# Optimization experiments

Measured on AMD Instinct MI355X. Metric: run time of the kernel, lower is better.

Reference implementation:

```python
import jax, jax.numpy as jnp
import numpy as np

ITER_NUM = 3       # nSteps of the SICE proximal loop (module iterNum)
NS_ITERS = 7       # Newton-Schulz iterations, hardcoded in _sice
F_LR = 5.0         # sice_lrate
F_SPARSITY = 0.07  # sparsity_val
BN_EPS = 1e-5


def _inv_sqrtm(x, iterN):
    """Batched Newton-Schulz inverse matrix square root (Sqrtm.forward)."""
    d = x.shape[-1]
    I3 = 3.0 * jnp.eye(d, dtype=x.dtype)
    normA = jnp.trace(x, axis1=-2, axis2=-1)            # [B]
    A = x / normA[:, None, None]
    ZY = 0.5 * (I3 - A)
    Y = A @ ZY
    Z = ZY
    for _ in range(iterN - 2):
        ZY = 0.5 * (I3 - Z @ Y)
        Y = Y @ ZY
        Z = ZY @ Z
    ZYZ = 0.5 * (I3 - Z @ Y) @ Z
    return ZYZ * (normA ** -0.5)[:, None, None]


def _covpool(x):
    """x: [B,C,H,W] -> centered second-order pooling [B,C,C] (Covpool)."""
    b, c, h, w = x.shape
    m = h * w
    xf = x.reshape(b, c, m)
    xc = xf - xf.mean(axis=-1, keepdims=True)
    # x @ I_hat @ x^T == (x - mean)(x - mean)^T / M
    return (xc @ xc.transpose(0, 2, 1)) / m


def _sice(x, jitter):
    C = _covpool(x)
    C = C / jnp.trace(C, axis1=-2, axis2=-1)[:, None, None]
    Ij = jnp.diag(1e-10 + 1e-9 * jitter)[None].astype(C.dtype)   # [1,D,D]
    zz = _inv_sqrtm(C + Ij, NS_ITERS)
    LLT = zz @ zz                                                # inv covariance init
    sym_C = 0.5 * (C + C.transpose(0, 2, 1))
    for i in range(ITER_NUM):
        Lp = jax.nn.relu(LLT)
        Lm = jax.nn.relu(-LLT)
        zz = _inv_sqrtm(LLT + Ij, NS_ITERS)
        g12 = -(zz @ zz) + sym_C
        dec = F_LR * (1.0 - i / (ITER_NUM - 1.0))
        Lp = jax.nn.relu(Lp - dec * (g12 + F_SPARSITY))
        Lm = jax.nn.relu(Lm - dec * (-g12 + F_SPARSITY))
        LLT = Lp - Lm
        LLT = 0.5 * (LLT + LLT.transpose(0, 2, 1))
    return LLT / jnp.sqrt(jnp.trace(LLT, axis1=-2, axis2=-1))[:, None, None]


def reference(x, conv_w, gamma, beta, jitter):
    # 1x1 conv dimension reduction + BatchNorm (batch stats, train mode) + ReLU
    y = jnp.einsum('bchw,dc->bdhw', x, conv_w)
    mu = y.mean(axis=(0, 2, 3), keepdims=True)
    var = y.var(axis=(0, 2, 3), keepdims=True)
    y = (y - mu) / jnp.sqrt(var + BN_EPS)
    y = jax.nn.relu(y * gamma[None, :, None, None] + beta[None, :, None, None])
    out = _sice(y, jitter)                                       # [B,D,D]
    b, d = out.shape[0], out.shape[1]
    iu = np.nonzero(np.triu(np.ones((d, d))).reshape(-1))[0]     # Triuvec indices
    return out.reshape(b, d * d)[:, iu]                          # [B, D*(D+1)/2]


def setup_inputs() -> dict:
    key = jax.random.key(0)
    k1, k2, k3 = jax.random.split(key, 3)
    B, CIN, H, W, DR = 32, 2048, 28, 28, 256
    x = jax.random.normal(k1, (B, CIN, H, W), dtype=jnp.float32)
    # kaiming normal, mode=fan_out (fan_out = DR*1*1): std = sqrt(2/DR)
    conv_w = jax.random.normal(k2, (DR, CIN), dtype=jnp.float32) * np.sqrt(2.0 / DR).astype(np.float32)
    gamma = jnp.ones((DR,), dtype=jnp.float32)
    beta = jnp.zeros((DR,), dtype=jnp.float32)
    jitter = jax.random.uniform(k3, (DR,), dtype=jnp.float32)
    return {"x": x, "conv_w": conv_w, "gamma": gamma, "beta": beta, "jitter": jitter}
```

## Files before the change

### kernel.cpp

```cpp
#include <hip/hip_runtime.h>
#include <utility>


typedef unsigned short u16;
typedef __attribute__((ext_vector_type(8))) __bf16 bf16x8;
typedef __attribute__((ext_vector_type(8))) _Float16 f16x8;
typedef __attribute__((ext_vector_type(4))) float f32x4;

#define DEV __device__ __forceinline__

DEV u16 f2bf(float f) {
  unsigned x = __float_as_uint(f);
  x += 0x7fffu + ((x >> 16) & 1u);
  return (u16)(x >> 16);
}
DEV float bf2f(u16 h) { return __uint_as_float(((unsigned)h) << 16); }

#define SB_SUM   0
#define SB_SSQ   256
#define SB_IJ    512
#define SB_TRC   768
#define SB_TR2   800
#define SB_TR3   832
#define SB_TRL   864
#define SB_DEN   896
#define SB_IJSUM 928

__global__ __launch_bounds__(256) void k_prep(const float* __restrict__ w,
                                              const float* __restrict__ jitter,
                                              _Float16* __restrict__ w_half,
                                              float* __restrict__ sb) {
  int gid = blockIdx.x * 256 + threadIdx.x;
  if (gid < 256 * 2048) w_half[gid] = (_Float16)w[gid];
  if (blockIdx.x == 0) {
    int t = threadIdx.x;
    float ij = 1e-10f + 1e-9f * jitter[t];
    sb[SB_IJ + t] = ij;
    if (t < 160) sb[SB_TRC + t] = 0.f;
    __shared__ float red[256];
    red[t] = ij; __syncthreads();
    for (int off = 128; off > 0; off >>= 1) {
      if (t < off) red[t] += red[t + off];
      __syncthreads();
    }
    if (t == 0) sb[SB_IJSUM] = red[0];
  }
}

__global__ __launch_bounds__(256) void k_conv(const _Float16* __restrict__ w_half,
                                              const float* __restrict__ x,
                                              _Float16* __restrict__ y) {
  int xb = blockIdx.x;
  int b = xb & 31;
  int rest = xb >> 5;
  int mt = rest / 13, ht = rest % 13;
  int hw0 = ht * 64;
  int t = threadIdx.x;
  int wv = t >> 6, lane = t & 63, m = lane & 15, quad = lane >> 4;
  __shared__ _Float16 lsA[2][128 * 40];
  __shared__ _Float16 lsB[2][64 * 40];
  f32x4 acc[4][2];
#pragma unroll
  for (int i = 0; i < 4; ++i)
#pragma unroll
    for (int j = 0; j < 2; ++j) acc[i][j] = (f32x4){0.f, 0.f, 0.f, 0.f};
  int rowA = t & 127, halfA = t >> 7;
  const _Float16* wp = w_half + ((size_t)(mt * 128 + rowA)) * 2048 + halfA * 16;
  int hwB = t & 63, cg = t >> 6;
  bool okB = (hw0 + hwB) < 784;
  const float* xp = x + ((size_t)b * 2048 + cg * 8) * 784 + hw0 + hwB;
  uint4 ra0, ra1;
  float rb[8];
  ra0 = *(const uint4*)(wp);
  ra1 = *(const uint4*)(wp + 8);
#pragma unroll
  for (int j = 0; j < 8; ++j) rb[j] = okB ? xp[(size_t)j * 784] : 0.f;
  int wr = (wv >> 1) * 64, wc = (wv & 1) * 32;
  for (int kc = 0; kc < 64; ++kc) {
    int buf = kc & 1;
    int loA = rowA * 40 + halfA * 16;
    *(uint4*)&lsA[buf][loA] = ra0;
    *(uint4*)&lsA[buf][loA + 8] = ra1;
    {
      union { f16x8 h; uint4 u; } pk;
#pragma unroll
      for (int j = 0; j < 8; ++j) pk.h[j] = (_Float16)rb[j];
      *(uint4*)&lsB[buf][hwB * 40 + cg * 8] = pk.u;
    }
    if (kc < 63) {
      int k0 = (kc + 1) * 32;
      ra0 = *(const uint4*)(wp + k0);
      ra1 = *(const uint4*)(wp + k0 + 8);
#pragma unroll
      for (int j = 0; j < 8; ++j)
        rb[j] = okB ? xp[((size_t)k0 + j) * 784] : 0.f;
    }
    __syncthreads();
    f16x8 af[4], bfg[2];
#pragma unroll
    for (int i = 0; i < 4; ++i)
      af[i] = *(const f16x8*)&lsA[buf][(wr + i * 16 + m) * 40 + quad * 8];
#pragma unroll
    for (int j = 0; j < 2; ++j)
      bfg[j] = *(const f16x8*)&lsB[buf][(wc + j * 16 + m) * 40 + quad * 8];
#pragma unroll
    for (int i = 0; i < 4; ++i)
#pragma unroll
      for (int j = 0; j < 2; ++j)
        acc[i][j] = __builtin_amdgcn_mfma_f32_16x16x32_f16(af[i], bfg[j], acc[i][j], 0, 0, 0);
  }
#pragma unroll
  for (int i = 0; i < 4; ++i)
#pragma unroll
    for (int j = 0; j < 2; ++j)
#pragma unroll
      for (int r = 0; r < 4; ++r) {
        int R = mt * 128 + wr + i * 16 + quad * 4 + r;
        int hwc = hw0 + wc + j * 16 + m;
        if (hwc < 784) y[((size_t)b * 256 + R) * 784 + hwc] = (_Float16)acc[i][j][r];
      }
}

__global__ __launch_bounds__(256) void k_stats(const _Float16* __restrict__ y,
                                               float* __restrict__ sb) {
  int d = blockIdx.x, t = threadIdx.x;
  float s = 0.f, q = 0.f;
  if (t < 196) {
    for (int b = 0; b < 32; ++b) {
      const _Float16* row = y + ((size_t)b * 256 + d) * 784;
      union { uint2 u; _Float16 h[4]; } v;
      v.u = *(const uint2*)(row + t * 4);
#pragma unroll
      for (int k = 0; k < 4; ++k) {
        float f = (float)v.h[k];
        s += f; q += f * f;
      }
    }
  }
  __shared__ float rs[256], rq[256];
  rs[t] = s; rq[t] = q; __syncthreads();
  for (int off = 128; off > 0; off >>= 1) {
    if (t < off) { rs[t] += rs[t + off]; rq[t] += rq[t + off]; }
    __syncthreads();
  }
  if (t == 0) { sb[SB_SUM + d] = rs[0]; sb[SB_SSQ + d] = rq[0]; }
}

__global__ __launch_bounds__(256) void k_bnapply(const _Float16* __restrict__ y,
                                                 const float* __restrict__ gamma,
                                                 const float* __restrict__ beta,
                                                 const float* __restrict__ sb,
                                                 _Float16* __restrict__ yc) {
  int xb = blockIdx.x;
  int d = xb >> 5, b = xb & 31, t = threadIdx.x;
  float mu = sb[SB_SUM + d] * (1.0f / 25088.0f);
  float var = sb[SB_SSQ + d] * (1.0f / 25088.0f) - mu * mu;
  float sc = gamma[d] / sqrtf(var + 1e-5f);
  float sh = beta[d] - mu * sc;
  const _Float16* row = y + ((size_t)b * 256 + d) * 784;
  float v[4];
  float s = 0.f;
#pragma unroll
  for (int i = 0; i < 4; ++i) {
    int idx = t + i * 256;
    float u = 0.f;
    if (idx < 784) u = fmaxf((float)row[idx] * sc + sh, 0.f);
    v[i] = u; s += u;
  }
  __shared__ float red[256];
  red[t] = s; __syncthreads();
  for (int off = 128; off > 0; off >>= 1) {
    if (t < off) red[t] += red[t + off];
    __syncthreads();
  }
  float mean = red[0] * (1.0f / 784.0f);
  _Float16* out = yc + ((size_t)b * 256 + d) * 800;
#pragma unroll
  for (int i = 0; i < 4; ++i) {
    int idx = t + i * 256;
    if (idx < 784) out[idx] = (_Float16)(v[i] - mean);
  }
  if (t < 16) out[784 + t] = (_Float16)0.f;
}

__global__ __launch_bounds__(256) void k_gram(const _Float16* __restrict__ yc,
                                              float* __restrict__ C,
                                              float* __restrict__ sb) {
  int xb = blockIdx.x;
  int b = xb & 31, rest = xb >> 5;
  int tr = rest >> 2, tc = rest & 3;
  int t = threadIdx.x, wv = t >> 6, lane = t & 63, m = lane & 15, quad = lane >> 4;
  __shared__ _Float16 lsA[2][32 * 40];
  __shared__ _Float16 lsB[2][64 * 40];
  f32x4 acc[2];
  acc[0] = (f32x4){0.f, 0.f, 0.f, 0.f};
  acc[1] = (f32x4){0.f, 0.f, 0.f, 0.f};
  int row = t >> 2, seg = t & 3;
  const _Float16* base = yc + (size_t)b * 256 * 800;
  const _Float16* Bp = base + (size_t)(tc * 64 + row) * 800 + seg * 8;
  const _Float16* Ap = base + (size_t)(tr * 32 + row) * 800 + seg * 8;
  bool doA = row < 32;
  uint4 rB = *(const uint4*)(Bp);
  uint4 rA = doA ? *(const uint4*)(Ap) : (uint4){0, 0, 0, 0};
  int ar = (wv >> 1) * 16, bcl = (wv & 1) * 32;
  for (int ks = 0; ks < 25; ++ks) {
    int buf = ks & 1;
    int lo = row * 40 + seg * 8;
    *(uint4*)&lsB[buf][lo] = rB;
    if (doA) *(uint4*)&lsA[buf][lo] = rA;
    if (ks < 24) {
      int k0 = (ks + 1) * 32;
      rB = *(const uint4*)(Bp + k0);
      if (doA) rA = *(const uint4*)(Ap + k0);
    }
    __syncthreads();
    f16x8 a0 = *(const f16x8*)&lsA[buf][(ar + m) * 40 + quad * 8];
    f16x8 b0 = *(const f16x8*)&lsB[buf][(bcl + m) * 40 + quad * 8];
    f16x8 b1 = *(const f16x8*)&lsB[buf][(bcl + 16 + m) * 40 + quad * 8];
    acc[0] = __builtin_amdgcn_mfma_f32_16x16x32_f16(a0, b0, acc[0], 0, 0, 0);
    acc[1] = __builtin_amdgcn_mfma_f32_16x16x32_f16(a0, b1, acc[1], 0, 0, 0);
  }
  const float inv = 1.0f / 784.0f;
#pragma unroll
  for (int j = 0; j < 2; ++j)
#pragma unroll
    for (int r = 0; r < 4; ++r) {
      int R = tr * 32 + ar + quad * 4 + r;
      int Cc = tc * 64 + bcl + j * 16 + m;
      float v = acc[j][r] * inv;
      C[((size_t)b * 256 + R) * 256 + Cc] = v;
      if (R == Cc) atomicAdd(&sb[SB_TRC + b], v);
    }
}

__global__ __launch_bounds__(256) void k_prepAZY(const float* __restrict__ src,
                                                 float* __restrict__ symC,
                                                 u16* __restrict__ Ah, u16* __restrict__ Al,
                                                 u16* __restrict__ ZYh, u16* __restrict__ ZYl,
                                                 float* __restrict__ sb, int slot, int mode) {
  int xb = blockIdx.x;
  int ig = xb >> 5, b = xb & 31, j = threadIdx.x;
  float trv = (mode == 0) ? 1.0f : sb[slot + b];
  float denom = trv + sb[SB_IJSUM];
  if (ig == 0 && j == 0) sb[SB_DEN + b] = denom;
  float trC = (mode == 0) ? sb[SB_TRC + b] : 1.0f;
#pragma unroll
  for (int ii = 0; ii < 8; ++ii) {
    int i = ig * 8 + ii;
    size_t idx = ((size_t)b * 256 + i) * 256 + j;
    float v;
    if (mode == 0) {
      float vij = src[idx] / trC;
      float vji = src[((size_t)b * 256 + j) * 256 + i] / trC;
      symC[idx] = 0.5f * (vij + vji);
      v = vij;
    } else {
      v = src[idx];
    }
    if (i == j) v += sb[SB_IJ + i];
    float A = v / denom;
    u16 h = f2bf(A);
    Ah[idx] = h; Al[idx] = f2bf(A - bf2f(h));
    float zy = 0.5f * ((i == j ? 3.0f : 0.0f) - A);
    h = f2bf(zy);
    ZYh[idx] = h; ZYl[idx] = f2bf(zy - bf2f(h));
  }
}

struct MMArgs {
  const u16* Ah; const u16* Al; const u16* Bh;
  u16* Oh; u16* Ol; float* Of; float* tr; int emode;
};

__global__ __launch_bounds__(256) void mm_ns(MMArgs g0, MMArgs g1,
                                             const float* __restrict__ sb) {
  int xb = blockIdx.x;
  int b = xb & 31;
  int rest = xb >> 5;
  MMArgs g = (rest < 32) ? g0 : g1;
  int tile = rest & 31;
  int tr = tile >> 2, tc = tile & 3;
  int t = threadIdx.x, wv = t >> 6, lane = t & 63, m = lane & 15, quad = lane >> 4;
  __shared__ u16 lsAh[2][32 * 40], lsAl[2][32 * 40];
  __shared__ u16 lsBh[2][64 * 40];
  f32x4 acc[2];
  acc[0] = (f32x4){0.f, 0.f, 0.f, 0.f};
  acc[1] = (f32x4){0.f, 0.f, 0.f, 0.f};
  int row = t >> 2, seg = t & 3;
  size_t mb = (size_t)b * 65536;
  size_t bO = mb + (size_t)(tc * 64 + row) * 256 + seg * 8;
  size_t aO = mb + (size_t)(tr * 32 + row) * 256 + seg * 8;
  bool doA = row < 32;
  uint4 rBh = *(const uint4*)(g.Bh + bO);
  uint4 rAh = doA ? *(const uint4*)(g.Ah + aO) : (uint4){0, 0, 0, 0};
  uint4 rAl = doA ? *(const uint4*)(g.Al + aO) : (uint4){0, 0, 0, 0};
  int ar = (wv >> 1) * 16, bcl = (wv & 1) * 32;
  for (int ks = 0; ks < 8; ++ks) {
    int buf = ks & 1;
    int lo = row * 40 + seg * 8;
    *(uint4*)&lsBh[buf][lo] = rBh;
    if (doA) {
      *(uint4*)&lsAh[buf][lo] = rAh;
      *(uint4*)&lsAl[buf][lo] = rAl;
    }
    if (ks < 7) {
      int k0 = (ks + 1) * 32;
      rBh = *(const uint4*)(g.Bh + bO + k0);
      if (doA) {
        rAh = *(const uint4*)(g.Ah + aO + k0);
        rAl = *(const uint4*)(g.Al + aO + k0);
      }
    }
    __syncthreads();
    bf16x8 ah = *(const bf16x8*)&lsAh[buf][(ar + m) * 40 + quad * 8];
    bf16x8 al = *(const bf16x8*)&lsAl[buf][(ar + m) * 40 + quad * 8];
    bf16x8 bh0 = *(const bf16x8*)&lsBh[buf][(bcl + m) * 40 + quad * 8];
    bf16x8 bh1 = *(const bf16x8*)&lsBh[buf][(bcl + 16 + m) * 40 + quad * 8];
    acc[0] = __builtin_amdgcn_mfma_f32_16x16x32_bf16(ah, bh0, acc[0], 0, 0, 0);
    acc[0] = __builtin_amdgcn_mfma_f32_16x16x32_bf16(al, bh0, acc[0], 0, 0, 0);
    acc[1] = __builtin_amdgcn_mfma_f32_16x16x32_bf16(ah, bh1, acc[1], 0, 0, 0);
    acc[1] = __builtin_amdgcn_mfma_f32_16x16x32_bf16(al, bh1, acc[1], 0, 0, 0);
  }
  float scl = 1.0f;
  if (g.emode == 2) scl = 1.0f / sqrtf(sb[SB_DEN + b]);
#pragma unroll
  for (int j = 0; j < 2; ++j)
#pragma unroll
    for (int r = 0; r < 4; ++r) {
      int R = tr * 32 + ar + quad * 4 + r;
      int Cc = tc * 64 + bcl + j * 16 + m;
      float v = acc[j][r];
      if (g.emode == 1) v = 0.5f * ((R == Cc ? 3.0f : 0.0f) - v);
      else if (g.emode == 2) v = v * scl;
      size_t oidx = mb + (size_t)R * 256 + Cc;
      if (g.emode == 3) {
        g.Of[oidx] = v;
        if (R == Cc && g.tr) atomicAdd(g.tr + b, v);
      } else {
        u16 h = f2bf(v);
        g.Oh[oidx] = h;
        g.Ol[oidx] = f2bf(v - bf2f(h));
      }
    }
}

__global__ __launch_bounds__(256) void k_sice(const float* __restrict__ LLT,
                                              const float* __restrict__ P,
                                              const float* __restrict__ symC,
                                              float* __restrict__ out,
                                              float* __restrict__ sb, int slot,
                                              float dec) {
  int xb = blockIdx.x;
  int b = xb & 31, p = xb >> 5;
  const int TRt[10] = {0, 0, 0, 0, 1, 1, 1, 2, 2, 3};
  const int TCt[10] = {0, 1, 2, 3, 1, 2, 3, 2, 3, 3};
  int tr = TRt[p], tc = TCt[p];
  __shared__ float ft[64][65];
  __shared__ float ot[64][65];
  int t = threadIdx.x;
  size_t base = (size_t)b * 65536;
#pragma unroll 4
  for (int it = 0; it < 16; ++it) {
    int idx = it * 256 + t;
    int r = idx >> 6, c = idx & 63;
    size_t o = base + (size_t)(tc * 64 + r) * 256 + tr * 64 + c;
    float L = LLT[o];
    float g = symC[o] - P[o];
    float f = fmaxf(fmaxf(L, 0.f) - dec * (g + 0.07f), 0.f) -
              fmaxf(fmaxf(-L, 0.f) - dec * (-g + 0.07f), 0.f);
    ft[r][c] = f;
  }
  __syncthreads();
  float tsum = 0.f;
#pragma unroll 4
  for (int it = 0; it < 16; ++it) {
    int idx = it * 256 + t;
    int r = idx >> 6, c = idx & 63;
    size_t o = base + (size_t)(tr * 64 + r) * 256 + tc * 64 + c;
    float L = LLT[o];
    float g = symC[o] - P[o];
    float f = fmaxf(fmaxf(L, 0.f) - dec * (g + 0.07f), 0.f) -
              fmaxf(fmaxf(-L, 0.f) - dec * (-g + 0.07f), 0.f);
    float val = 0.5f * (f + ft[c][r]);
    out[o] = val;
    ot[r][c] = val;
    if (tr == tc && r == c) tsum += val;
  }
  if (tr == tc) {
    if (tsum != 0.f) atomicAdd(&sb[slot + b], tsum);
  } else {
    __syncthreads();
#pragma unroll 4
    for (int it = 0; it < 16; ++it) {
      int idx = it * 256 + t;
      int r = idx >> 6, c = idx & 63;
      size_t o = base + (size_t)(tc * 64 + r) * 256 + tr * 64 + c;
      out[o] = ot[c][r];
    }
  }
}

__global__ __launch_bounds__(256) void k_out(const float* __restrict__ LLT,
                                             const float* __restrict__ sb,
                                             float* __restrict__ out) {
  int xb = blockIdx.x;
  int i = xb >> 5, b = xb & 31, j = threadIdx.x;
  if (j < i) return;
  float inv = 1.0f / sqrtf(sb[SB_TRL + b]);
  int tl = i * 256 - (i * (i - 1)) / 2 + (j - i);
  out[(size_t)b * 32896 + tl] = LLT[((size_t)b * 256 + i) * 256 + j] * inv;
}

extern "C" void kernel_launch(void* const* d_in, const int* in_sizes, int n_in,
                              void* d_out, int out_size, void* d_ws, size_t ws_size,
                              hipStream_t stream) {
  const float* x = (const float*)d_in[0];
  const float* w = (const float*)d_in[1];
  const float* gamma = (const float*)d_in[2];
  const float* beta = (const float*)d_in[3];
  const float* jitter = (const float*)d_in[4];
  char* ws = (char*)d_ws;

  _Float16* w_half = (_Float16*)(ws + 0);
  float* sb = (float*)(ws + (1 << 20));
  _Float16* y = (_Float16*)(ws + (2 << 20));
  _Float16* yc = (_Float16*)(ws + (16 << 20));
  char* ov = ws + (32 << 20);
  float* Craw = (float*)(ov + 0);
  float* symC = (float*)(ov + 8388608);
  float* LLTa = (float*)(ov + 16777216);
  float* P = (float*)(ov + 25165824);
  float* LLTb = (float*)(ov + 33554432);
  u16* bf[12];
  for (int i = 0; i < 12; ++i) bf[i] = (u16*)(ov + 41943040 + (size_t)i * 4194304);

  k_prep<<<2048, 256, 0, stream>>>(w, jitter, w_half, sb);
  k_conv<<<832, 256, 0, stream>>>(w_half, x, y);
  k_stats<<<256, 256, 0, stream>>>(y, sb);
  k_bnapply<<<8192, 256, 0, stream>>>(y, gamma, beta, sb, yc);
  k_gram<<<1024, 256, 0, stream>>>(yc, Craw, sb);

  auto run_ns = [&](const float* src, int mode, int slot_in, float* Pout,
                    float* tr_out) {
    k_prepAZY<<<1024, 256, 0, stream>>>(src, symC, bf[0], bf[1], bf[2], bf[3], sb, slot_in, mode);
    u16 *Ah = bf[0], *Al = bf[1], *ZYh = bf[2], *ZYl = bf[3];
    u16 *Yh = bf[4], *Yl = bf[5], *Z2h = bf[6], *Z2l = bf[7];
    u16 *Th = bf[8], *Tl = bf[9], *zzh = bf[10], *zzl = bf[11];
    MMArgs m1{Ah, Al, ZYh, Yh, Yl, nullptr, nullptr, 0};
    mm_ns<<<1024, 256, 0, stream>>>(m1, m1, sb);
    u16 *Ych = Yh, *Ycl = Yl, *Yah = Ah, *Yal = Al;
    u16 *Zch = ZYh, *Zcl = ZYl, *Zah = Z2h, *Zal = Z2l;
    for (int it = 0; it < 5; ++it) {
      MMArgs mt{Zch, Zcl, Ych, Th, Tl, nullptr, nullptr, 1};
      mm_ns<<<1024, 256, 0, stream>>>(mt, mt, sb);
      MMArgs my{Ych, Ycl, Th, Yah, Yal, nullptr, nullptr, 0};
      MMArgs mz{Th, Tl, Zch, Zah, Zal, nullptr, nullptr, 0};
      mm_ns<<<2048, 256, 0, stream>>>(my, mz, sb);
      std::swap(Ych, Yah); std::swap(Ycl, Yal);
      std::swap(Zch, Zah); std::swap(Zcl, Zal);
    }
    MMArgs mt6{Zch, Zcl, Ych, Th, Tl, nullptr, nullptr, 1};
    mm_ns<<<1024, 256, 0, stream>>>(mt6, mt6, sb);
    MMArgs mz7{Th, Tl, Zch, zzh, zzl, nullptr, nullptr, 2};
    mm_ns<<<1024, 256, 0, stream>>>(mz7, mz7, sb);
    MMArgs mzz{zzh, zzl, zzh, nullptr, nullptr, Pout, tr_out, 3};
    mm_ns<<<1024, 256, 0, stream>>>(mzz, mzz, sb);
  };

  run_ns(Craw, 0, 0, LLTa, sb + SB_TR2);
  run_ns(LLTa, 1, SB_TR2, P, nullptr);
  k_sice<<<320, 256, 0, stream>>>(LLTa, P, symC, LLTb, sb, SB_TR3, 5.0f);
  run_ns(LLTb, 1, SB_TR3, P, nullptr);
  k_sice<<<320, 256, 0, stream>>>(LLTb, P, symC, LLTa, sb, SB_TRL, 2.5f);

  k_out<<<8192, 256, 0, stream>>>(LLTa, sb, (float*)d_out);
}
```

Measured before the change: 878.4 us.

## Exploit symmetry in Gram and NS matmuls; split-K conv with fused reduce-stats

The Gram kernel and every Newton-Schulz matmul now compute only the 20 upper-triangular 32x64 tiles per batch (instead of 32) and mirror results via a shared-memory transpose. This relies on the products being symmetric, which holds for commuting polynomial iterates of a symmetric matrix. The conv is restructured as split-K over four 512-channel chunks with full 256-row tiles, writing fp32 partials. A new reduce kernel sums the partials, writes fp16 y and atomically accumulates the BN statistics. This adds extra partial-sum traffic in exchange for more conv parallelism and less matmul work.

```diff
diff --git a/kernel.cpp b/kernel.cpp
--- a/kernel.cpp
+++ b/kernel.cpp
@@ -34,6 +34,8 @@
   if (gid < 256 * 2048) w_half[gid] = (_Float16)w[gid];
   if (blockIdx.x == 0) {
     int t = threadIdx.x;
+    sb[SB_SUM + t] = 0.f;
+    sb[SB_SSQ + t] = 0.f;
     float ij = 1e-10f + 1e-9f * jitter[t];
     sb[SB_IJ + t] = ij;
     if (t < 160) sb[SB_TRC + t] = 0.f;
@@ -49,92 +51,93 @@
 
 __global__ __launch_bounds__(256) void k_conv(const _Float16* __restrict__ w_half,
                                               const float* __restrict__ x,
-                                              _Float16* __restrict__ y) {
+                                              float* __restrict__ yp) {
   int xb = blockIdx.x;
   int b = xb & 31;
   int rest = xb >> 5;
-  int mt = rest / 13, ht = rest % 13;
+  int kc = rest / 13, ht = rest % 13;
   int hw0 = ht * 64;
+  int kbase = kc * 512;
   int t = threadIdx.x;
   int wv = t >> 6, lane = t & 63, m = lane & 15, quad = lane >> 4;
-  __shared__ _Float16 lsA[2][128 * 40];
-  __shared__ _Float16 lsB[2][64 * 40];
-  f32x4 acc[4][2];
+  __shared__ _Float16 lsA[256 * 40];
+  __shared__ _Float16 lsB[64 * 40];
+  f32x4 acc[4][4];
 #pragma unroll
   for (int i = 0; i < 4; ++i)
 #pragma unroll
-    for (int j = 0; j < 2; ++j) acc[i][j] = (f32x4){0.f, 0.f, 0.f, 0.f};
-  int rowA = t & 127, halfA = t >> 7;
-  const _Float16* wp = w_half + ((size_t)(mt * 128 + rowA)) * 2048 + halfA * 16;
+    for (int j = 0; j < 4; ++j) acc[i][j] = (f32x4){0.f, 0.f, 0.f, 0.f};
+  const _Float16* wp = w_half + (size_t)t * 2048 + kbase;
   int hwB = t & 63, cg = t >> 6;
   bool okB = (hw0 + hwB) < 784;
-  const float* xp = x + ((size_t)b * 2048 + cg * 8) * 784 + hw0 + hwB;
-  uint4 ra0, ra1;
+  const float* xp = x + ((size_t)b * 2048 + kbase + cg * 8) * 784 + hw0 + hwB;
+  uint4 ra[4];
   float rb[8];
-  ra0 = *(const uint4*)(wp);
-  ra1 = *(const uint4*)(wp + 8);
+#pragma unroll
+  for (int s = 0; s < 4; ++s) ra[s] = *(const uint4*)(wp + s * 8);
 #pragma unroll
   for (int j = 0; j < 8; ++j) rb[j] = okB ? xp[(size_t)j * 784] : 0.f;
-  int wr = (wv >> 1) * 64, wc = (wv & 1) * 32;
-  for (int kc = 0; kc < 64; ++kc) {
-    int buf = kc & 1;
-    int loA = rowA * 40 + halfA * 16;
-    *(uint4*)&lsA[buf][loA] = ra0;
-    *(uint4*)&lsA[buf][loA + 8] = ra1;
+  for (int it = 0; it < 16; ++it) {
+    if (it) __syncthreads();
+#pragma unroll
+    for (int s = 0; s < 4; ++s) *(uint4*)&lsA[t * 40 + s * 8] = ra[s];
     {
       union { f16x8 h; uint4 u; } pk;
 #pragma unroll
       for (int j = 0; j < 8; ++j) pk.h[j] = (_Float16)rb[j];
-      *(uint4*)&lsB[buf][hwB * 40 + cg * 8] = pk.u;
-    }
-    if (kc < 63) {
-      int k0 = (kc + 1) * 32;
-      ra0 = *(const uint4*)(wp + k0);
-      ra1 = *(const uint4*)(wp + k0 + 8);
+      *(uint4*)&lsB[hwB * 40 + cg * 8] = pk.u;
+    }
+    __syncthreads();
+    if (it < 15) {
+      int k0 = (it + 1) * 32;
+#pragma unroll
+      for (int s = 0; s < 4; ++s) ra[s] = *(const uint4*)(wp + k0 + s * 8);
 #pragma unroll
       for (int j = 0; j < 8; ++j)
         rb[j] = okB ? xp[((size_t)k0 + j) * 784] : 0.f;
     }
-    __syncthreads();
-    f16x8 af[4], bfg[2];
+    f16x8 af[4], bfg[4];
 #pragma unroll
     for (int i = 0; i < 4; ++i)
-      af[i] = *(const f16x8*)&lsA[buf][(wr + i * 16 + m) * 40 + quad * 8];
-#pragma unroll
-    for (int j = 0; j < 2; ++j)
-      bfg[j] = *(const f16x8*)&lsB[buf][(wc + j * 16 + m) * 40 + quad * 8];
+      af[i] = *(const f16x8*)&lsA[(wv * 64 + i * 16 + m) * 40 + quad * 8];
+#pragma unroll
+    for (int j = 0; j < 4; ++j)
+      bfg[j] = *(const f16x8*)&lsB[(j * 16 + m) * 40 + quad * 8];
 #pragma unroll
     for (int i = 0; i < 4; ++i)
 #pragma unroll
-      for (int j = 0; j < 2; ++j)
+      for (int j = 0; j < 4; ++j)
         acc[i][j] = __builtin_amdgcn_mfma_f32_16x16x32_f16(af[i], bfg[j], acc[i][j], 0, 0, 0);
   }
+  float* out = yp + (size_t)(kc * 32 + b) * 256 * 784;
 #pragma unroll
   for (int i = 0; i < 4; ++i)
 #pragma unroll
-    for (int j = 0; j < 2; ++j)
+    for (int j = 0; j < 4; ++j)
 #pragma unroll
       for (int r = 0; r < 4; ++r) {
-        int R = mt * 128 + wr + i * 16 + quad * 4 + r;
-        int hwc = hw0 + wc + j * 16 + m;
-        if (hwc < 784) y[((size_t)b * 256 + R) * 784 + hwc] = (_Float16)acc[i][j][r];
+        int R = wv * 64 + i * 16 + quad * 4 + r;
+        int hwc = hw0 + j * 16 + m;
+        if (hwc < 784) out[(size_t)R * 784 + hwc] = acc[i][j][r];
       }
 }
 
-__global__ __launch_bounds__(256) void k_stats(const _Float16* __restrict__ y,
-                                               float* __restrict__ sb) {
-  int d = blockIdx.x, t = threadIdx.x;
+__global__ __launch_bounds__(256) void k_red(const float* __restrict__ yp,
+                                             _Float16* __restrict__ y,
+                                             float* __restrict__ sb) {
+  int xb = blockIdx.x;
+  int b = xb & 31, d = xb >> 5, t = threadIdx.x;
+  const size_t cs = (size_t)32 * 256 * 784;
+  const float* p = yp + ((size_t)b * 256 + d) * 784;
+  _Float16* yo = y + ((size_t)b * 256 + d) * 784;
   float s = 0.f, q = 0.f;
-  if (t < 196) {
-    for (int b = 0; b < 32; ++b) {
-      const _Float16* row = y + ((size_t)b * 256 + d) * 784;
-      union { uint2 u; _Float16 h[4]; } v;
-      v.u = *(const uint2*)(row + t * 4);
-#pragma unroll
-      for (int k = 0; k < 4; ++k) {
-        float f = (float)v.h[k];
-        s += f; q += f * f;
-      }
+#pragma unroll
+  for (int it = 0; it < 4; ++it) {
+    int idx = it * 256 + t;
+    if (idx < 784) {
+      float v = p[idx] + p[cs + idx] + p[2 * cs + idx] + p[3 * cs + idx];
+      yo[idx] = (_Float16)v;
+      s += v; q += v * v;
     }
   }
   __shared__ float rs[256], rq[256];
@@ -143,7 +146,10 @@
     if (t < off) { rs[t] += rs[t + off]; rq[t] += rq[t + off]; }
     __syncthreads();
   }
-  if (t == 0) { sb[SB_SUM + d] = rs[0]; sb[SB_SSQ + d] = rq[0]; }
+  if (t == 0) {
+    atomicAdd(&sb[SB_SUM + d], rs[0]);
+    atomicAdd(&sb[SB_SSQ + d], rq[0]);
+  }
 }
 
 __global__ __launch_bounds__(256) void k_bnapply(const _Float16* __restrict__ y,
@@ -183,15 +189,19 @@
   if (t < 16) out[784 + t] = (_Float16)0.f;
 }
 
+__device__ __constant__ signed char SYM_TR[20] = {0,1,2,3,4,5,6,7, 2,3,4,5,6,7, 4,5,6,7, 6,7};
+__device__ __constant__ signed char SYM_TC[20] = {0,0,0,0,0,0,0,0, 1,1,1,1,1,1, 2,2,2,2, 3,3};
+
 __global__ __launch_bounds__(256) void k_gram(const _Float16* __restrict__ yc,
                                               float* __restrict__ C,
                                               float* __restrict__ sb) {
   int xb = blockIdx.x;
-  int b = xb & 31, rest = xb >> 5;
-  int tr = rest >> 2, tc = rest & 3;
+  int b = xb & 31, p = xb >> 5;
+  int tr = SYM_TR[p], tc = SYM_TC[p];
   int t = threadIdx.x, wv = t >> 6, lane = t & 63, m = lane & 15, quad = lane >> 4;
   __shared__ _Float16 lsA[2][32 * 40];
   __shared__ _Float16 lsB[2][64 * 40];
+  __shared__ float lsT[32][65];
   f32x4 acc[2];
   acc[0] = (f32x4){0.f, 0.f, 0.f, 0.f};
   acc[1] = (f32x4){0.f, 0.f, 0.f, 0.f};
@@ -221,16 +231,30 @@
     acc[1] = __builtin_amdgcn_mfma_f32_16x16x32_f16(a0, b1, acc[1], 0, 0, 0);
   }
   const float inv = 1.0f / 784.0f;
+  float* Cb = C + (size_t)b * 65536;
 #pragma unroll
   for (int j = 0; j < 2; ++j)
 #pragma unroll
     for (int r = 0; r < 4; ++r) {
-      int R = tr * 32 + ar + quad * 4 + r;
-      int Cc = tc * 64 + bcl + j * 16 + m;
+      int rl = ar + quad * 4 + r, cl = bcl + j * 16 + m;
+      int R = tr * 32 + rl, Cc = tc * 64 + cl;
       float v = acc[j][r] * inv;
-      C[((size_t)b * 256 + R) * 256 + Cc] = v;
+      Cb[(size_t)R * 256 + Cc] = v;
+      lsT[rl][cl] = v;
       if (R == Cc) atomicAdd(&sb[SB_TRC + b], v);
     }
+  __syncthreads();
+  int tcm2 = 2 * (tr >> 1);
+#pragma unroll
+  for (int it = 0; it < 8; ++it) {
+    int idx = it * 256 + t;
+    int r2 = idx & 31, c2 = idx >> 5;
+    int trm = 2 * tc + (c2 >> 5);
+    if (trm < tcm2) {
+      int Rm = 64 * tc + c2, Cm = 32 * tr + r2;
+      Cb[(size_t)Rm * 256 + Cm] = lsT[r2][c2];
+    }
+  }
 }
 
 __global__ __launch_bounds__(256) void k_prepAZY(const float* __restrict__ src,
@@ -277,12 +301,13 @@
   int xb = blockIdx.x;
   int b = xb & 31;
   int rest = xb >> 5;
-  MMArgs g = (rest < 32) ? g0 : g1;
-  int tile = rest & 31;
-  int tr = tile >> 2, tc = tile & 3;
+  MMArgs g = (rest < 20) ? g0 : g1;
+  int p = (rest < 20) ? rest : rest - 20;
+  int tr = SYM_TR[p], tc = SYM_TC[p];
   int t = threadIdx.x, wv = t >> 6, lane = t & 63, m = lane & 15, quad = lane >> 4;
   __shared__ u16 lsAh[2][32 * 40], lsAl[2][32 * 40];
   __shared__ u16 lsBh[2][64 * 40];
+  __shared__ float lsT[32][65];
   f32x4 acc[2];
   acc[0] = (f32x4){0.f, 0.f, 0.f, 0.f};
   acc[1] = (f32x4){0.f, 0.f, 0.f, 0.f};
@@ -327,11 +352,12 @@
   for (int j = 0; j < 2; ++j)
 #pragma unroll
     for (int r = 0; r < 4; ++r) {
-      int R = tr * 32 + ar + quad * 4 + r;
-      int Cc = tc * 64 + bcl + j * 16 + m;
+      int rl = ar + quad * 4 + r, cl = bcl + j * 16 + m;
+      int R = tr * 32 + rl, Cc = tc * 64 + cl;
       float v = acc[j][r];
       if (g.emode == 1) v = 0.5f * ((R == Cc ? 3.0f : 0.0f) - v);
       else if (g.emode == 2) v = v * scl;
+      lsT[rl][cl] = v;
       size_t oidx = mb + (size_t)R * 256 + Cc;
       if (g.emode == 3) {
         g.Of[oidx] = v;
@@ -342,6 +368,26 @@
         g.Ol[oidx] = f2bf(v - bf2f(h));
       }
     }
+  __syncthreads();
+  int tcm2 = 2 * (tr >> 1);
+#pragma unroll
+  for (int it = 0; it < 8; ++it) {
+    int idx = it * 256 + t;
+    int r2 = idx & 31, c2 = idx >> 5;
+    int trm = 2 * tc + (c2 >> 5);
+    if (trm < tcm2) {
+      int Rm = 64 * tc + c2, Cm = 32 * tr + r2;
+      size_t oidx = mb + (size_t)Rm * 256 + Cm;
+      float v = lsT[r2][c2];
+      if (g.emode == 3) {
+        g.Of[oidx] = v;
+      } else {
+        u16 h = f2bf(v);
+        g.Oh[oidx] = h;
+        g.Ol[oidx] = f2bf(v - bf2f(h));
+      }
+    }
+  }
 }
 
 __global__ __launch_bounds__(256) void k_sice(const float* __restrict__ LLT,
@@ -426,6 +472,7 @@
   _Float16* y = (_Float16*)(ws + (2 << 20));
   _Float16* yc = (_Float16*)(ws + (16 << 20));
   char* ov = ws + (32 << 20);
+  float* yp = (float*)(ov);
   float* Craw = (float*)(ov + 0);
   float* symC = (float*)(ov + 8388608);
   float* LLTa = (float*)(ov + 16777216);
@@ -435,10 +482,10 @@
   for (int i = 0; i < 12; ++i) bf[i] = (u16*)(ov + 41943040 + (size_t)i * 4194304);
 
   k_prep<<<2048, 256, 0, stream>>>(w, jitter, w_half, sb);
-  k_conv<<<832, 256, 0, stream>>>(w_half, x, y);
-  k_stats<<<256, 256, 0, stream>>>(y, sb);
+  k_conv<<<1664, 256, 0, stream>>>(w_half, x, yp);
+  k_red<<<8192, 256, 0, stream>>>(yp, y, sb);
   k_bnapply<<<8192, 256, 0, stream>>>(y, gamma, beta, sb, yc);
-  k_gram<<<1024, 256, 0, stream>>>(yc, Craw, sb);
+  k_gram<<<640, 256, 0, stream>>>(yc, Craw, sb);
 
   auto run_ns = [&](const float* src, int mode, int slot_in, float* Pout,
                     float* tr_out) {
@@ -447,24 +494,24 @@
     u16 *Yh = bf[4], *Yl = bf[5], *Z2h = bf[6], *Z2l = bf[7];
     u16 *Th = bf[8], *Tl = bf[9], *zzh = bf[10], *zzl = bf[11];
     MMArgs m1{Ah, Al, ZYh, Yh, Yl, nullptr, nullptr, 0};
-    mm_ns<<<1024, 256, 0, stream>>>(m1, m1, sb);
+    mm_ns<<<640, 256, 0, stream>>>(m1, m1, sb);
     u16 *Ych = Yh, *Ycl = Yl, *Yah = Ah, *Yal = Al;
     u16 *Zch = ZYh, *Zcl = ZYl, *Zah = Z2h, *Zal = Z2l;
     for (int it = 0; it < 5; ++it) {
       MMArgs mt{Zch, Zcl, Ych, Th, Tl, nullptr, nullptr, 1};
-      mm_ns<<<1024, 256, 0, stream>>>(mt, mt, sb);
+      mm_ns<<<640, 256, 0, stream>>>(mt, mt, sb);
       MMArgs my{Ych, Ycl, Th, Yah, Yal, nullptr, nullptr, 0};
       MMArgs mz{Th, Tl, Zch, Zah, Zal, nullptr, nullptr, 0};
-      mm_ns<<<2048, 256, 0, stream>>>(my, mz, sb);
+      mm_ns<<<1280, 256, 0, stream>>>(my, mz, sb);
       std::swap(Ych, Yah); std::swap(Ycl, Yal);
       std::swap(Zch, Zah); std::swap(Zcl, Zal);
     }
     MMArgs mt6{Zch, Zcl, Ych, Th, Tl, nullptr, nullptr, 1};
-    mm_ns<<<1024, 256, 0, stream>>>(mt6, mt6, sb);
+    mm_ns<<<640, 256, 0, stream>>>(mt6, mt6, sb);
     MMArgs mz7{Th, Tl, Zch, zzh, zzl, nullptr, nullptr, 2};
-    mm_ns<<<1024, 256, 0, stream>>>(mz7, mz7, sb);
+    mm_ns<<<640, 256, 0, stream>>>(mz7, mz7, sb);
     MMArgs mzz{zzh, zzl, zzh, nullptr, nullptr, Pout, tr_out, 3};
-    mm_ns<<<1024, 256, 0, stream>>>(mzz, mzz, sb);
+    mm_ns<<<640, 256, 0, stream>>>(mzz, mzz, sb);
   };
 
   run_ns(Craw, 0, 0, LLTa, sb + SB_TR2);
```

Result: slower. 1.004 ms (+14.2%).

## Fuse weight fp16 conversion into conv and shrink conv tile to 64x64

Applied to the files above, without the earlier changes.

The separate weight fp32-to-fp16 conversion pass is removed, and the conv kernel now reads fp32 weights and converts them in registers before staging to LDS. The conv tile shrinks from 128x64 to 64x64, doubling the block count to 1664, and the prefetch depth grows to two k-chunks. This trades higher x re-reads (each x tile is now loaded for four d-tiles instead of two) and less per-wave MFMA reuse for more blocks, deeper latency hiding and one fewer kernel launch.

```diff
diff --git a/kernel.cpp b/kernel.cpp
--- a/kernel.cpp
+++ b/kernel.cpp
@@ -26,99 +26,91 @@
 #define SB_DEN   896
 #define SB_IJSUM 928
 
-__global__ __launch_bounds__(256) void k_prep(const float* __restrict__ w,
-                                              const float* __restrict__ jitter,
-                                              _Float16* __restrict__ w_half,
+__global__ __launch_bounds__(256) void k_prep(const float* __restrict__ jitter,
                                               float* __restrict__ sb) {
-  int gid = blockIdx.x * 256 + threadIdx.x;
-  if (gid < 256 * 2048) w_half[gid] = (_Float16)w[gid];
-  if (blockIdx.x == 0) {
-    int t = threadIdx.x;
-    float ij = 1e-10f + 1e-9f * jitter[t];
-    sb[SB_IJ + t] = ij;
-    if (t < 160) sb[SB_TRC + t] = 0.f;
-    __shared__ float red[256];
-    red[t] = ij; __syncthreads();
-    for (int off = 128; off > 0; off >>= 1) {
-      if (t < off) red[t] += red[t + off];
-      __syncthreads();
-    }
-    if (t == 0) sb[SB_IJSUM] = red[0];
-  }
-}
-
-__global__ __launch_bounds__(256) void k_conv(const _Float16* __restrict__ w_half,
+  int t = threadIdx.x;
+  float ij = 1e-10f + 1e-9f * jitter[t];
+  sb[SB_IJ + t] = ij;
+  if (t < 160) sb[SB_TRC + t] = 0.f;
+  __shared__ float red[256];
+  red[t] = ij; __syncthreads();
+  for (int off = 128; off > 0; off >>= 1) {
+    if (t < off) red[t] += red[t + off];
+    __syncthreads();
+  }
+  if (t == 0) sb[SB_IJSUM] = red[0];
+}
+
+__global__ __launch_bounds__(256) void k_conv(const float* __restrict__ w,
                                               const float* __restrict__ x,
                                               _Float16* __restrict__ y) {
   int xb = blockIdx.x;
   int b = xb & 31;
   int rest = xb >> 5;
   int mt = rest / 13, ht = rest % 13;
-  int hw0 = ht * 64;
+  int d0 = mt * 64, hw0 = ht * 64;
   int t = threadIdx.x;
   int wv = t >> 6, lane = t & 63, m = lane & 15, quad = lane >> 4;
-  __shared__ _Float16 lsA[2][128 * 40];
+  __shared__ _Float16 lsA[2][64 * 40];
   __shared__ _Float16 lsB[2][64 * 40];
-  f32x4 acc[4][2];
-#pragma unroll
-  for (int i = 0; i < 4; ++i)
-#pragma unroll
-    for (int j = 0; j < 2; ++j) acc[i][j] = (f32x4){0.f, 0.f, 0.f, 0.f};
-  int rowA = t & 127, halfA = t >> 7;
-  const _Float16* wp = w_half + ((size_t)(mt * 128 + rowA)) * 2048 + halfA * 16;
+  f32x4 acc[4];
+#pragma unroll
+  for (int j = 0; j < 4; ++j) acc[j] = (f32x4){0.f, 0.f, 0.f, 0.f};
+  int rowA = t >> 2, segA = t & 3;
+  const float* wp = w + (size_t)(d0 + rowA) * 2048 + segA * 8;
   int hwB = t & 63, cg = t >> 6;
   bool okB = (hw0 + hwB) < 784;
   const float* xp = x + ((size_t)b * 2048 + cg * 8) * 784 + hw0 + hwB;
-  uint4 ra0, ra1;
-  float rb[8];
-  ra0 = *(const uint4*)(wp);
-  ra1 = *(const uint4*)(wp + 8);
-#pragma unroll
-  for (int j = 0; j < 8; ++j) rb[j] = okB ? xp[(size_t)j * 784] : 0.f;
-  int wr = (wv >> 1) * 64, wc = (wv & 1) * 32;
+  float4 qa[2][2];
+  float qb[2][8];
+#pragma unroll
+  for (int pf = 0; pf < 2; ++pf) {
+    int k0 = pf * 32;
+    qa[pf][0] = *(const float4*)(wp + k0);
+    qa[pf][1] = *(const float4*)(wp + k0 + 4);
+#pragma unroll
+    for (int j = 0; j < 8; ++j)
+      qb[pf][j] = okB ? xp[((size_t)k0 + j) * 784] : 0.f;
+  }
   for (int kc = 0; kc < 64; ++kc) {
     int buf = kc & 1;
-    int loA = rowA * 40 + halfA * 16;
-    *(uint4*)&lsA[buf][loA] = ra0;
-    *(uint4*)&lsA[buf][loA + 8] = ra1;
     {
-      union { f16x8 h; uint4 u; } pk;
-#pragma unroll
-      for (int j = 0; j < 8; ++j) pk.h[j] = (_Float16)rb[j];
-      *(uint4*)&lsB[buf][hwB * 40 + cg * 8] = pk.u;
-    }
-    if (kc < 63) {
-      int k0 = (kc + 1) * 32;
-      ra0 = *(const uint4*)(wp + k0);
-      ra1 = *(const uint4*)(wp + k0 + 8);
+      union { f16x8 h; uint4 u; } pa;
+#pragma unroll
+      for (int s = 0; s < 4; ++s) {
+        pa.h[s] = (_Float16)((&qa[buf][0].x)[s]);
+        pa.h[4 + s] = (_Float16)((&qa[buf][1].x)[s]);
+      }
+      *(uint4*)&lsA[buf][rowA * 40 + segA * 8] = pa.u;
+      union { f16x8 h; uint4 u; } pb;
+#pragma unroll
+      for (int j = 0; j < 8; ++j) pb.h[j] = (_Float16)qb[buf][j];
+      *(uint4*)&lsB[buf][hwB * 40 + cg * 8] = pb.u;
+    }
+    if (kc < 62) {
+      int k0 = (kc + 2) * 32;
+      qa[buf][0] = *(const float4*)(wp + k0);
+      qa[buf][1] = *(const float4*)(wp + k0 + 4);
 #pragma unroll
       for (int j = 0; j < 8; ++j)
-        rb[j] = okB ? xp[((size_t)k0 + j) * 784] : 0.f;
-    }
-    __syncthreads();
-    f16x8 af[4], bfg[2];
-#pragma unroll
-    for (int i = 0; i < 4; ++i)
-      af[i] = *(const f16x8*)&lsA[buf][(wr + i * 16 + m) * 40 + quad * 8];
-#pragma unroll
-    for (int j = 0; j < 2; ++j)
-      bfg[j] = *(const f16x8*)&lsB[buf][(wc + j * 16 + m) * 40 + quad * 8];
-#pragma unroll
-    for (int i = 0; i < 4; ++i)
-#pragma unroll
-      for (int j = 0; j < 2; ++j)
-        acc[i][j] = __builtin_amdgcn_mfma_f32_16x16x32_f16(af[i], bfg[j], acc[i][j], 0, 0, 0);
-  }
-#pragma unroll
-  for (int i = 0; i < 4; ++i)
-#pragma unroll
-    for (int j = 0; j < 2; ++j)
-#pragma unroll
-      for (int r = 0; r < 4; ++r) {
-        int R = mt * 128 + wr + i * 16 + quad * 4 + r;
-        int hwc = hw0 + wc + j * 16 + m;
-        if (hwc < 784) y[((size_t)b * 256 + R) * 784 + hwc] = (_Float16)acc[i][j][r];
-      }
+        qb[buf][j] = okB ? xp[((size_t)k0 + j) * 784] : 0.f;
+    }
+    __syncthreads();
+    f16x8 af = *(const f16x8*)&lsA[buf][(wv * 16 + m) * 40 + quad * 8];
+#pragma unroll
+    for (int j = 0; j < 4; ++j) {
+      f16x8 bfg = *(const f16x8*)&lsB[buf][(j * 16 + m) * 40 + quad * 8];
+      acc[j] = __builtin_amdgcn_mfma_f32_16x16x32_f16(af, bfg, acc[j], 0, 0, 0);
+    }
+  }
+#pragma unroll
+  for (int j = 0; j < 4; ++j)
+#pragma unroll
+    for (int r = 0; r < 4; ++r) {
+      int R = d0 + wv * 16 + quad * 4 + r;
+      int hwc = hw0 + j * 16 + m;
+      if (hwc < 784) y[((size_t)b * 256 + R) * 784 + hwc] = (_Float16)acc[j][r];
+    }
 }
 
 __global__ __launch_bounds__(256) void k_stats(const _Float16* __restrict__ y,
@@ -421,7 +413,6 @@
   const float* jitter = (const float*)d_in[4];
   char* ws = (char*)d_ws;
 
-  _Float16* w_half = (_Float16*)(ws + 0);
   float* sb = (float*)(ws + (1 << 20));
   _Float16* y = (_Float16*)(ws + (2 << 20));
   _Float16* yc = (_Float16*)(ws + (16 << 20));
@@ -434,8 +425,8 @@
   u16* bf[12];
   for (int i = 0; i < 12; ++i) bf[i] = (u16*)(ov + 41943040 + (size_t)i * 4194304);
 
-  k_prep<<<2048, 256, 0, stream>>>(w, jitter, w_half, sb);
-  k_conv<<<832, 256, 0, stream>>>(w_half, x, y);
+  k_prep<<<1, 256, 0, stream>>>(jitter, sb);
+  k_conv<<<1664, 256, 0, stream>>>(w, x, y);
   k_stats<<<256, 256, 0, stream>>>(y, sb);
   k_bnapply<<<8192, 256, 0, stream>>>(y, gamma, beta, sb, yc);
   k_gram<<<1024, 256, 0, stream>>>(yc, Craw, sb);
```

Measured after the change: 1.442 ms. 1.64x slower.
